# Optimization experiments

Hardware: AMD Instinct MI355X
Metric: run time of the kernel (lower is better)

## Reference

```python
import jax, jax.numpy as jnp
import numpy as np

N, E, B, D, NODE_DIM, REL = 50000, 800000, 500, 64, 6, 200
IN_FEAT = 3 * D + 2 * NODE_DIM  # 204


def _xavier(k, shape):
    fan_out, fan_in = shape
    lim = float(np.sqrt(6.0 / (fan_in + fan_out)))
    return jax.random.uniform(k, shape, jnp.float32, -lim, lim)


def setup_inputs() -> dict:
    key = jax.random.key(0)
    ks = jax.random.split(key, 8)
    x = jax.random.normal(ks[0], (N, NODE_DIM), jnp.float32)
    edge_index = jax.random.randint(ks[1], (2, E), 0, N, jnp.int32)
    edge_rel = jax.random.randint(ks[2], (E,), 0, REL, jnp.int32)
    batch = jnp.repeat(jnp.arange(B, dtype=jnp.int32), N // B)  # 100 nodes/graph
    mask = jnp.ones((E,), jnp.float32)
    edge_emb = jax.random.normal(ks[3], (REL, D), jnp.float32) * 0.02
    W0 = _xavier(ks[4], (D, IN_FEAT))
    W1 = _xavier(ks[5], (D, IN_FEAT))
    W2 = _xavier(ks[6], (D, IN_FEAT))
    b0 = jnp.zeros((D,), jnp.float32)
    b1 = jnp.zeros((D,), jnp.float32)
    b2 = jnp.zeros((D,), jnp.float32)
    return {"x": x, "edge_index": edge_index, "edge_rel": edge_rel, "batch": batch,
            "mask": mask, "edge_emb": edge_emb, "W0": W0, "b0": b0, "W1": W1,
            "b1": b1, "W2": W2, "b2": b2, "num_graphs": B}


def reference(x, edge_index, edge_rel, batch, mask, edge_emb, W0, b0, W1, b1, W2, b2, num_graphs):
    n_nodes = x.shape[0]
    row, col = edge_index[0], edge_index[1]
    # head/tail idxs: cumulative offsets of per-graph node counts
    num_per = jax.ops.segment_sum(jnp.ones_like(batch, jnp.float32), batch, num_segments=num_graphs)
    head_idxs = jnp.cumsum(jnp.concatenate([jnp.zeros(1, jnp.float32), num_per[:-1]])).astype(jnp.int32)
    tail_idxs = head_idxs + 1
    # zero x except head/tail rows
    x0 = jnp.zeros_like(x).at[head_idxs].set(x[head_idxs]).at[tail_idxs].set(x[tail_idxs])
    ea = edge_emb[edge_rel]  # [E, D]
    m = mask[:, None]
    for W, b in ((W0, b0), (W1, b1), (W2, b2)):
        agg = jax.ops.segment_sum(ea * m, col, num_segments=n_nodes)  # [N, D]
        cnt = jax.ops.segment_sum(m, col, num_segments=n_nodes)      # [N, 1]
        node_rep = jnp.concatenate([agg / (cnt + 1.0), x0], axis=1)  # [N, D+6]
        edge_rep = jnp.concatenate([node_rep[row], node_rep[col], ea], axis=-1)  # [E, 204]
        ea = jax.nn.relu(edge_rep @ W.T + b)  # PathCon edge_mlp + gnn_non_linear
    agg = jax.ops.segment_sum(ea * m, col, num_segments=n_nodes)
    cnt = jax.ops.segment_sum(m, col, num_segments=n_nodes)
    node_rep = agg / (cnt + 1.0)  # [N, D]
    pooled = jax.ops.segment_max(node_rep, batch, num_segments=num_graphs)  # 'max' readout
    graph_emb = jnp.concatenate([pooled, node_rep[head_idxs], node_rep[tail_idxs]], axis=1)
    return graph_emb, node_rep, ea
```

## Files before the change

kernel.cpp:

```cpp
#include <hip/hip_runtime.h>
#include <stdint.h>

typedef __attribute__((ext_vector_type(8))) short short8;
typedef __attribute__((ext_vector_type(4))) float f32x4;
typedef __attribute__((ext_vector_type(2))) unsigned int u32x2;

#define D_ 64
#define NODE_DIM_ 6
#define INF_ 204
#define EB 64
#define WEA_PER_LAYER 4096
#define WN_PER_LAYER 12288

__device__ __forceinline__ unsigned int f2bf(float f){
  uint32_t u = __float_as_uint(f);
  u += 0x7fffu + ((u >> 16) & 1u);
  return u >> 16;
}

__global__ void k_counts(const int* __restrict__ batch, const int* __restrict__ col,
                         int* __restrict__ counts, int* __restrict__ cnt, int N, int E){
  int i = blockIdx.x*256 + threadIdx.x;
  if (i < E) atomicAdd(&cnt[col[i]], 1);
  if (i < N) atomicAdd(&counts[batch[i]], 1);
}

__global__ void k_scans(const int* __restrict__ cnt, int* __restrict__ off, int Nn,
                        const int* __restrict__ counts, int* __restrict__ head, int B){
  __shared__ int s[1024];
  int t = threadIdx.x;
  const int CH = (Nn + 1024) / 1024;
  int base = t*CH;
  int sum = 0;
  for (int i = 0; i < CH; ++i){ int idx = base+i; if (idx < Nn) sum += cnt[idx]; }
  s[t] = sum;
  __syncthreads();
  for (int o = 1; o < 1024; o <<= 1){
    int u = (t >= o) ? s[t-o] : 0;
    __syncthreads();
    s[t] += u;
    __syncthreads();
  }
  int run = (t == 0) ? 0 : s[t-1];
  for (int i = 0; i < CH; ++i){
    int idx = base+i;
    if (idx <= Nn){ off[idx] = run; if (idx < Nn) run += cnt[idx]; }
  }
  __syncthreads();
  int v = (t < B) ? counts[t] : 0;
  s[t] = v;
  __syncthreads();
  for (int o = 1; o < 1024; o <<= 1){
    int u = (t >= o) ? s[t-o] : 0;
    __syncthreads();
    s[t] += u;
    __syncthreads();
  }
  if (t < B) head[t] = s[t] - v;
}

__global__ void k_fill(const int* __restrict__ row, const int* __restrict__ col,
                       const int* __restrict__ rel, const float* __restrict__ mask,
                       const int* __restrict__ off, int* __restrict__ fpos,
                       int* __restrict__ csr, int* __restrict__ rowp, int* __restrict__ colp,
                       int* __restrict__ relp, float* __restrict__ maskp, int E){
  int e = blockIdx.x*256 + threadIdx.x;
  if (e >= E) return;
  int c = col[e];
  int p = atomicAdd(&fpos[c], 1);
  int pos = off[c] + p;
  csr[pos]  = e;
  rowp[pos] = row[e];
  colp[pos] = c;
  relp[pos] = rel[e];
  maskp[pos]= mask[e];
}

__global__ void k_x0b(const int* __restrict__ head, const float* __restrict__ x,
                      float* __restrict__ x0b, int B){
  int idx = blockIdx.x*256 + threadIdx.x;
  if (idx >= B*2*NODE_DIM_) return;
  int g = idx / (2*NODE_DIM_);
  int j = idx % (2*NODE_DIM_);
  int node = head[g] + j / NODE_DIM_;
  int c = j % NODE_DIM_;
  x0b[(size_t)node*8 + c] = x[node*NODE_DIM_ + c];
}

__global__ void k_pack_w(const float* __restrict__ W0, const float* __restrict__ W1,
                         const float* __restrict__ W2,
                         unsigned short* __restrict__ Wea, unsigned short* __restrict__ Wn){
  int idx = blockIdx.x*256 + threadIdx.x;
  if (idx < 3*WEA_PER_LAYER){
    int l = idx / WEA_PER_LAYER;
    int rem = idx % WEA_PER_LAYER;
    const float* W = (l==0) ? W0 : ((l==1) ? W1 : W2);
    int i = rem & 7, s = rem >> 3;
    int lane = s & 63, t = s >> 6;
    int kc = t & 1, nt = t >> 1;
    int n = lane & 15, kg = lane >> 4;
    int k = kc*32 + kg*8 + i;
    int c = nt*16 + n;
    Wea[idx] = (unsigned short)f2bf(W[c*INF_ + 140 + k]);
    return;
  }
  int idx2 = idx - 3*WEA_PER_LAYER;
  if (idx2 >= 3*WN_PER_LAYER) return;
  int l = idx2 / WN_PER_LAYER;
  int rem = idx2 % WN_PER_LAYER;
  const float* W = (l==0) ? W0 : ((l==1) ? W1 : W2);
  int i = rem & 7, s = rem >> 3;
  int lane = s & 63, t = s >> 6;
  int kc = t % 3, nt = t / 3;
  int n = lane & 15, kg = lane >> 4;
  int k = kc*32 + kg*8 + i;
  int c = nt*16 + n;
  float v = 0.f;
  if (k < 70) v = (nt < 4) ? W[c*INF_ + k] : W[(c-64)*INF_ + 70 + k];
  Wn[idx2] = (unsigned short)f2bf(v);
}

__global__ void k_pack_emb(const float* __restrict__ emb, unsigned short* __restrict__ emb_bf, int n){
  int i = blockIdx.x*256 + threadIdx.x;
  if (i < n) emb_bf[i] = (unsigned short)f2bf(emb[i]);
}

__global__ __launch_bounds__(256) void k_agg0_inv(
    const float* __restrict__ emb, const int* __restrict__ relp,
    const int* __restrict__ off, const float* __restrict__ maskp,
    float* __restrict__ agg, float* __restrict__ inv, int Nn)
{
  int wid = (blockIdx.x*256 + threadIdx.x) >> 6;
  if (wid >= Nn) return;
  int lane = threadIdx.x & 63;
  int sub = lane >> 4, q = lane & 15;
  int s = off[wid], t = off[wid+1];
  float a0=0.f,a1=0.f,a2=0.f,a3=0.f, cs=0.f;
  for (int i = s; i < t; i += 4){
    int ii = i + sub;
    float mv = (ii < t) ? maskp[ii] : 0.f;
    int r = (ii < t) ? relp[ii] : 0;
    f32x4 v = *reinterpret_cast<const f32x4*>(&emb[r*D_ + q*4]);
    a0 += v.x*mv; a1 += v.y*mv; a2 += v.z*mv; a3 += v.w*mv;
    cs += mv;
  }
  a0 += __shfl_xor(a0,16); a1 += __shfl_xor(a1,16); a2 += __shfl_xor(a2,16);
  a3 += __shfl_xor(a3,16); cs += __shfl_xor(cs,16);
  a0 += __shfl_xor(a0,32); a1 += __shfl_xor(a1,32); a2 += __shfl_xor(a2,32);
  a3 += __shfl_xor(a3,32); cs += __shfl_xor(cs,32);
  if (sub == 0){
    float iv = 1.f/(cs + 1.f);
    f32x4 w = {a0*iv, a1*iv, a2*iv, a3*iv};
    *reinterpret_cast<f32x4*>(&agg[(size_t)wid*D_ + q*4]) = w;
    if (q == 0) inv[wid] = iv;
  }
}

__global__ __launch_bounds__(256) void k_ynode(
    const float* __restrict__ agg, const float* __restrict__ x0b,
    const unsigned short* __restrict__ Wn,
    const float* __restrict__ bias, float* __restrict__ Ybuf, int Nn)
{
  __shared__ __align__(16) short tile[32*104];
  int tid = threadIdx.x;
  int n0 = blockIdx.x*32;
  if (tid < 128){
    int e = tid >> 2, w = tid & 3;
    *reinterpret_cast<short8*>(&tile[e*104 + 72 + w*8]) = short8{0,0,0,0,0,0,0,0};
  }
  const f32x4* agg4 = reinterpret_cast<const f32x4*>(agg);
  const f32x4* x0b4 = reinterpret_cast<const f32x4*>(x0b);
  for (int s = tid; s < 32*18; s += 256){
    int e = s/18, q = s - e*18;
    f32x4 v = {0.f,0.f,0.f,0.f};
    if (n0 + e < Nn){
      if (q < 16) v = agg4[(size_t)(n0+e)*16 + q];
      else        v = x0b4[(size_t)(n0+e)*2 + (q-16)];
    }
    u32x2 pk;
    pk.x = f2bf(v.x) | (f2bf(v.y) << 16);
    pk.y = f2bf(v.z) | (f2bf(v.w) << 16);
    *reinterpret_cast<u32x2*>(&tile[e*104 + q*4]) = pk;
  }
  __syncthreads();
  int lane = tid & 63, wv = tid >> 6;
  int r16 = lane & 15, kg = lane >> 4;
  const short8* W8 = reinterpret_cast<const short8*>(Wn);
  f32x4 acc[2][2] = {};
  #pragma unroll
  for (int kc = 0; kc < 3; ++kc){
    short8 a0 = *reinterpret_cast<const short8*>(&tile[r16*104 + kc*32 + kg*8]);
    short8 a1 = *reinterpret_cast<const short8*>(&tile[(16+r16)*104 + kc*32 + kg*8]);
    #pragma unroll
    for (int t = 0; t < 2; ++t){
      int nt = wv*2 + t;
      short8 wf = W8[(nt*3 + kc)*64 + lane];
      acc[0][t] = __builtin_amdgcn_mfma_f32_16x16x32_bf16(a0, wf, acc[0][t], 0,0,0);
      acc[1][t] = __builtin_amdgcn_mfma_f32_16x16x32_bf16(a1, wf, acc[1][t], 0,0,0);
    }
  }
  #pragma unroll
  for (int t = 0; t < 2; ++t){
    int nt = wv*2 + t;
    int c = nt*16 + r16;
    float b = (nt < 4) ? bias[c] : 0.f;
    #pragma unroll
    for (int m = 0; m < 2; ++m)
      #pragma unroll
      for (int j = 0; j < 4; ++j){
        int node = n0 + m*16 + kg*4 + j;
        if (node < Nn) Ybuf[(size_t)node*128 + c] = acc[m][t][j] + b;
      }
  }
}

template<int FIRST, int FOUT>
__global__ __launch_bounds__(256) void k_gemm(
    const unsigned short* __restrict__ ea_bf, const unsigned short* __restrict__ emb_bf,
    const float* __restrict__ Ybuf,
    unsigned short* __restrict__ ea_out_bf, float* __restrict__ ea_out_f32,
    float* __restrict__ agg,
    const int* __restrict__ rowp, const int* __restrict__ colp,
    const int* __restrict__ relp, const int* __restrict__ csr,
    const float* __restrict__ maskp, const float* __restrict__ inv,
    const unsigned short* __restrict__ Wea, int E)
{
  __shared__ __align__(16) float stile[EB*68];
  __shared__ int s_row[EB], s_col[EB], s_rel[EB], s_csr[EB];
  __shared__ float s_mask[EB], s_inv[EB];
  int tid = threadIdx.x;
  int e0 = blockIdx.x*EB;
  if (tid < EB){
    int ge = e0 + tid;
    bool ok = ge < E;
    int cc = ok ? colp[ge] : 0;
    s_col[tid] = cc;
    s_row[tid] = ok ? rowp[ge] : 0;
    s_mask[tid]= ok ? maskp[ge] : 0.f;
    s_inv[tid] = inv[cc];
    if (FIRST) s_rel[tid] = ok ? relp[ge] : 0;
    if (FOUT)  s_csr[tid] = ok ? csr[ge] : 0;
  }
  __syncthreads();
  const f32x4* Yb4 = reinterpret_cast<const f32x4*>(Ybuf);
  f32x4* st4 = reinterpret_cast<f32x4*>(stile);
  #pragma unroll
  for (int h = 0; h < 4; ++h){
    int s = tid + h*256;
    int e = s >> 4, q = s & 15;
    f32x4 a = Yb4[(size_t)s_row[e]*32 + q];
    f32x4 b = Yb4[(size_t)s_col[e]*32 + 16 + q];
    st4[e*17 + q] = a + b;
  }
  int lane = tid & 63, wv = tid >> 6;
  int r16 = lane & 15, kg = lane >> 4;
  const short8* W8 = reinterpret_cast<const short8*>(Wea);
  short8 wf[4][2];
  #pragma unroll
  for (int nt = 0; nt < 4; ++nt)
    #pragma unroll
    for (int kc = 0; kc < 2; ++kc)
      wf[nt][kc] = W8[(nt*2 + kc)*64 + lane];
  f32x4 acc[4] = {};
  #pragma unroll
  for (int kc = 0; kc < 2; ++kc){
    short8 a;
    if (FIRST){
      a = *reinterpret_cast<const short8*>(&emb_bf[(size_t)s_rel[wv*16 + r16]*D_ + kc*32 + kg*8]);
    } else {
      int eA = e0 + wv*16 + r16; if (eA >= E) eA = E-1;
      a = *reinterpret_cast<const short8*>(&ea_bf[(size_t)eA*D_ + kc*32 + kg*8]);
    }
    #pragma unroll
    for (int nt = 0; nt < 4; ++nt)
      acc[nt] = __builtin_amdgcn_mfma_f32_16x16x32_bf16(a, wf[nt][kc], acc[nt], 0,0,0);
  }
  __syncthreads();
  float v[4][4];
  #pragma unroll
  for (int nt = 0; nt < 4; ++nt)
    #pragma unroll
    for (int j = 0; j < 4; ++j){
      int et = wv*16 + kg*4 + j;
      float x = acc[nt][j] + stile[et*68 + nt*16 + r16];
      v[nt][j] = x > 0.f ? x : 0.f;
    }
  __syncthreads();
  if (FOUT == 0){
    unsigned short* ob = reinterpret_cast<unsigned short*>(stile);
    #pragma unroll
    for (int nt = 0; nt < 4; ++nt)
      #pragma unroll
      for (int j = 0; j < 4; ++j)
        ob[(wv*16 + kg*4 + j)*72 + nt*16 + r16] = (unsigned short)f2bf(v[nt][j]);
    __syncthreads();
    #pragma unroll
    for (int h = 0; h < 2; ++h){
      int s = tid + h*256;
      int e = s >> 3, w = s & 7;
      int ge = e0 + e;
      if (ge < E)
        *reinterpret_cast<short8*>(&ea_out_bf[(size_t)ge*D_ + w*8]) =
          *reinterpret_cast<const short8*>(&ob[e*72 + w*8]);
    }
    {
      int c = tid & 63, g = tid >> 6;
      int base = g*16;
      int cur = s_col[base]; float civ = s_inv[base]; float run = 0.f;
      #pragma unroll
      for (int e = base; e < base+16; ++e){
        int col = s_col[e];
        if (col != cur){
          atomicAdd(&agg[(size_t)cur*D_ + c], run*civ);
          run = 0.f; cur = col; civ = s_inv[e];
        }
        float val = __uint_as_float((uint32_t)ob[e*72 + c] << 16);
        run += val * s_mask[e];
      }
      atomicAdd(&agg[(size_t)cur*D_ + c], run*civ);
    }
  } else {
    #pragma unroll
    for (int nt = 0; nt < 4; ++nt)
      #pragma unroll
      for (int j = 0; j < 4; ++j)
        stile[(wv*16 + kg*4 + j)*68 + nt*16 + r16] = v[nt][j];
    __syncthreads();
    f32x4* out4 = reinterpret_cast<f32x4*>(ea_out_f32);
    #pragma unroll
    for (int h = 0; h < 4; ++h){
      int s = tid + h*256;
      int e = s >> 4, q = s & 15;
      int ge = e0 + e;
      if (ge < E) out4[(size_t)s_csr[e]*16 + q] = st4[e*17 + q];
    }
    {
      int c = tid & 63, g = tid >> 6;
      int base = g*16;
      int cur = s_col[base]; float civ = s_inv[base]; float run = 0.f;
      #pragma unroll
      for (int e = base; e < base+16; ++e){
        int col = s_col[e];
        if (col != cur){
          atomicAdd(&agg[(size_t)cur*D_ + c], run*civ);
          run = 0.f; cur = col; civ = s_inv[e];
        }
        run += stile[e*68 + c] * s_mask[e];
      }
      atomicAdd(&agg[(size_t)cur*D_ + c], run*civ);
    }
  }
}

__global__ void k_pool(const float* __restrict__ nrep_out, const int* __restrict__ head,
                       const int* __restrict__ counts, float* __restrict__ gout, int B){
  __shared__ float s[4][64];
  int g = blockIdx.x;
  int lane = threadIdx.x & 63, sub = threadIdx.x >> 6;
  int h = head[g]; int n = counts[g];
  float m = -3.402823466e38f;
  for (int i = sub; i < n; i += 4)
    m = fmaxf(m, nrep_out[(size_t)(h+i)*D_ + lane]);
  s[sub][lane] = m;
  __syncthreads();
  if (sub == 0){
    m = fmaxf(fmaxf(s[0][lane], s[1][lane]), fmaxf(s[2][lane], s[3][lane]));
    gout[(size_t)g*192 + lane]       = m;
    gout[(size_t)g*192 + 64  + lane] = nrep_out[(size_t)h*D_ + lane];
    gout[(size_t)g*192 + 128 + lane] = nrep_out[(size_t)(h+1)*D_ + lane];
  }
}

extern "C" void kernel_launch(void* const* d_in, const int* in_sizes, int n_in,
                              void* d_out, int out_size, void* d_ws, size_t ws_size,
                              hipStream_t stream)
{
  const float* x    = (const float*)d_in[0];
  const int*   eidx = (const int*)d_in[1];
  const int*   erel = (const int*)d_in[2];
  const int*   batch= (const int*)d_in[3];
  const float* mask = (const float*)d_in[4];
  const float* emb  = (const float*)d_in[5];
  const float* W0   = (const float*)d_in[6];
  const float* b0   = (const float*)d_in[7];
  const float* W1   = (const float*)d_in[8];
  const float* b1   = (const float*)d_in[9];
  const float* W2   = (const float*)d_in[10];
  const float* b2   = (const float*)d_in[11];

  int N = in_sizes[0] / NODE_DIM_;
  int E = in_sizes[2];
  int B = (int)(((long long)out_size - (long long)N*D_ - (long long)E*D_) / 192);

  float* out_ge   = (float*)d_out;
  float* out_nrep = out_ge + (size_t)B*192;
  float* out_ea   = out_nrep + (size_t)N*D_;

  char* w = (char*)d_ws;
  auto alloc = [&](size_t bytes)->char*{ char* p = w; w += (bytes + 255) & ~(size_t)255; return p; };
  unsigned short* ea_p = (unsigned short*)alloc((size_t)E*D_*2);
  float* Ybuf   = (float*)alloc((size_t)N*128*4);
  float* aggP   = (float*)alloc((size_t)N*D_*4);
  float* aggQ   = (float*)alloc((size_t)N*D_*4);
  float* x0b    = (float*)alloc((size_t)N*8*4);
  float* invb   = (float*)alloc((size_t)N*4);
  int*   cnt_i  = (int*)  alloc((size_t)N*4);
  int*   off    = (int*)  alloc((size_t)(N+1)*4);
  int*   fpos   = (int*)  alloc((size_t)N*4);
  int*   csr    = (int*)  alloc((size_t)E*4);
  int*   rowp   = (int*)  alloc((size_t)E*4);
  int*   colp   = (int*)  alloc((size_t)E*4);
  int*   relp   = (int*)  alloc((size_t)E*4);
  float* maskp  = (float*)alloc((size_t)E*4);
  int*   counts = (int*)  alloc((size_t)B*4);
  int*   head   = (int*)  alloc((size_t)B*4);
  unsigned short* Wea = (unsigned short*)alloc((size_t)3*WEA_PER_LAYER*2);
  unsigned short* Wn  = (unsigned short*)alloc((size_t)3*WN_PER_LAYER*2);
  unsigned short* emb_bf = (unsigned short*)alloc((size_t)200*D_*2 + 256);

  hipMemsetAsync(cnt_i,  0, (size_t)N*4, stream);
  hipMemsetAsync(fpos,   0, (size_t)N*4, stream);
  hipMemsetAsync(counts, 0, (size_t)B*4, stream);
  hipMemsetAsync(x0b,    0, (size_t)N*8*4, stream);
  hipMemsetAsync(aggQ,   0, (size_t)N*D_*4, stream);

  const int* erow = eidx;
  const int* ecol = eidx + E;

  k_counts   <<<(E+255)/256, 256, 0, stream>>>(batch, ecol, counts, cnt_i, N, E);
  k_scans    <<<1, 1024, 0, stream>>>(cnt_i, off, N, counts, head, B);
  k_x0b      <<<(B*2*NODE_DIM_+255)/256, 256, 0, stream>>>(head, x, x0b, B);
  k_fill     <<<(E+255)/256, 256, 0, stream>>>(erow, ecol, erel, mask, off, fpos,
                                               csr, rowp, colp, relp, maskp, E);
  k_pack_w   <<<(3*(WEA_PER_LAYER+WN_PER_LAYER)+255)/256, 256, 0, stream>>>(W0, W1, W2, Wea, Wn);
  k_pack_emb <<<(200*D_+255)/256, 256, 0, stream>>>(emb, emb_bf, 200*D_);

  int nblk_g = (E + EB - 1) / EB;
  int nblk_a = (N + 3) / 4;
  int nblk_y = (N + 31) / 32;

  k_agg0_inv<<<nblk_a, 256, 0, stream>>>(emb, relp, off, maskp, aggP, invb, N);
  k_ynode<<<nblk_y, 256, 0, stream>>>(aggP, x0b, Wn, b0, Ybuf, N);
  k_gemm<1,0><<<nblk_g, 256, 0, stream>>>(ea_p, emb_bf, Ybuf, ea_p, out_ea, aggQ,
                                          rowp, colp, relp, csr, maskp, invb, Wea, E);
  hipMemsetAsync(aggP, 0, (size_t)N*D_*4, stream);
  k_ynode<<<nblk_y, 256, 0, stream>>>(aggQ, x0b, Wn + WN_PER_LAYER, b1, Ybuf, N);
  k_gemm<0,0><<<nblk_g, 256, 0, stream>>>(ea_p, emb_bf, Ybuf, ea_p, out_ea, aggP,
                                          rowp, colp, relp, csr, maskp, invb,
                                          Wea + WEA_PER_LAYER, E);
  hipMemsetAsync(out_nrep, 0, (size_t)N*D_*4, stream);
  k_ynode<<<nblk_y, 256, 0, stream>>>(aggP, x0b, Wn + 2*WN_PER_LAYER, b2, Ybuf, N);
  k_gemm<0,1><<<nblk_g, 256, 0, stream>>>(ea_p, emb_bf, Ybuf, ea_p, out_ea, out_nrep,
                                          rowp, colp, relp, csr, maskp, invb,
                                          Wea + 2*WEA_PER_LAYER, E);

  k_pool<<<B, 256, 0, stream>>>(out_nrep, head, counts, out_ge, B);
}
```

Measured before the change: 785.1 us.

## Pack per-edge CSR metadata into int4 records and merge small setup kernels

```diff
diff --git a/kernel.cpp b/kernel.cpp
--- a/kernel.cpp
+++ b/kernel.cpp
@@ -26,7 +26,8 @@
 }
 
 __global__ void k_scans(const int* __restrict__ cnt, int* __restrict__ off, int Nn,
-                        const int* __restrict__ counts, int* __restrict__ head, int B){
+                        const int* __restrict__ counts, int* __restrict__ head, int B,
+                        const float* __restrict__ x, float* __restrict__ x0b){
   __shared__ int s[1024];
   int t = threadIdx.x;
   const int CH = (Nn + 1024) / 1024;
@@ -57,39 +58,30 @@
     __syncthreads();
   }
   if (t < B) head[t] = s[t] - v;
+  __syncthreads();
+  for (int idx = t; idx < B*2*NODE_DIM_; idx += 1024){
+    int g = idx / (2*NODE_DIM_);
+    int j = idx % (2*NODE_DIM_);
+    int node = (s[g] - counts[g]) + j / NODE_DIM_;
+    int c = j % NODE_DIM_;
+    x0b[(size_t)node*8 + c] = x[node*NODE_DIM_ + c];
+  }
 }
 
 __global__ void k_fill(const int* __restrict__ row, const int* __restrict__ col,
                        const int* __restrict__ rel, const float* __restrict__ mask,
-                       const int* __restrict__ off, int* __restrict__ fpos,
-                       int* __restrict__ csr, int* __restrict__ rowp, int* __restrict__ colp,
-                       int* __restrict__ relp, float* __restrict__ maskp, int E){
+                       int* __restrict__ fpos, int4* __restrict__ e4, int E){
   int e = blockIdx.x*256 + threadIdx.x;
   if (e >= E) return;
   int c = col[e];
-  int p = atomicAdd(&fpos[c], 1);
-  int pos = off[c] + p;
-  csr[pos]  = e;
-  rowp[pos] = row[e];
-  colp[pos] = c;
-  relp[pos] = rel[e];
-  maskp[pos]= mask[e];
-}
-
-__global__ void k_x0b(const int* __restrict__ head, const float* __restrict__ x,
-                      float* __restrict__ x0b, int B){
-  int idx = blockIdx.x*256 + threadIdx.x;
-  if (idx >= B*2*NODE_DIM_) return;
-  int g = idx / (2*NODE_DIM_);
-  int j = idx % (2*NODE_DIM_);
-  int node = head[g] + j / NODE_DIM_;
-  int c = j % NODE_DIM_;
-  x0b[(size_t)node*8 + c] = x[node*NODE_DIM_ + c];
-}
-
-__global__ void k_pack_w(const float* __restrict__ W0, const float* __restrict__ W1,
-                         const float* __restrict__ W2,
-                         unsigned short* __restrict__ Wea, unsigned short* __restrict__ Wn){
+  int pos = atomicAdd(&fpos[c], 1);
+  e4[pos] = make_int4(row[e], c, (e << 8) | rel[e], __float_as_int(mask[e]));
+}
+
+__global__ void k_pack(const float* __restrict__ W0, const float* __restrict__ W1,
+                       const float* __restrict__ W2, const float* __restrict__ emb,
+                       unsigned short* __restrict__ Wea, unsigned short* __restrict__ Wn,
+                       unsigned short* __restrict__ emb_bf){
   int idx = blockIdx.x*256 + threadIdx.x;
   if (idx < 3*WEA_PER_LAYER){
     int l = idx / WEA_PER_LAYER;
@@ -105,42 +97,41 @@
     return;
   }
   int idx2 = idx - 3*WEA_PER_LAYER;
-  if (idx2 >= 3*WN_PER_LAYER) return;
-  int l = idx2 / WN_PER_LAYER;
-  int rem = idx2 % WN_PER_LAYER;
-  const float* W = (l==0) ? W0 : ((l==1) ? W1 : W2);
-  int i = rem & 7, s = rem >> 3;
-  int lane = s & 63, t = s >> 6;
-  int kc = t % 3, nt = t / 3;
-  int n = lane & 15, kg = lane >> 4;
-  int k = kc*32 + kg*8 + i;
-  int c = nt*16 + n;
-  float v = 0.f;
-  if (k < 70) v = (nt < 4) ? W[c*INF_ + k] : W[(c-64)*INF_ + 70 + k];
-  Wn[idx2] = (unsigned short)f2bf(v);
-}
-
-__global__ void k_pack_emb(const float* __restrict__ emb, unsigned short* __restrict__ emb_bf, int n){
-  int i = blockIdx.x*256 + threadIdx.x;
-  if (i < n) emb_bf[i] = (unsigned short)f2bf(emb[i]);
+  if (idx2 < 3*WN_PER_LAYER){
+    int l = idx2 / WN_PER_LAYER;
+    int rem = idx2 % WN_PER_LAYER;
+    const float* W = (l==0) ? W0 : ((l==1) ? W1 : W2);
+    int i = rem & 7, s = rem >> 3;
+    int lane = s & 63, t = s >> 6;
+    int kc = t % 3, nt = t / 3;
+    int n = lane & 15, kg = lane >> 4;
+    int k = kc*32 + kg*8 + i;
+    int c = nt*16 + n;
+    float v = 0.f;
+    if (k < 70) v = (nt < 4) ? W[c*INF_ + k] : W[(c-64)*INF_ + 70 + k];
+    Wn[idx2] = (unsigned short)f2bf(v);
+    return;
+  }
+  int idx3 = idx2 - 3*WN_PER_LAYER;
+  if (idx3 < 200*D_) emb_bf[idx3] = (unsigned short)f2bf(emb[idx3]);
 }
 
 __global__ __launch_bounds__(256) void k_agg0_inv(
-    const float* __restrict__ emb, const int* __restrict__ relp,
-    const int* __restrict__ off, const float* __restrict__ maskp,
-    float* __restrict__ agg, float* __restrict__ inv, int Nn)
+    const float* __restrict__ emb, const int4* __restrict__ e4,
+    const int* __restrict__ off, float* __restrict__ agg,
+    float* __restrict__ inv, int Nn)
 {
   int wid = (blockIdx.x*256 + threadIdx.x) >> 6;
   if (wid >= Nn) return;
   int lane = threadIdx.x & 63;
-  int sub = lane >> 4, q = lane & 15;
+  int sub = lane >> 4, ch = lane & 15;
   int s = off[wid], t = off[wid+1];
   float a0=0.f,a1=0.f,a2=0.f,a3=0.f, cs=0.f;
   for (int i = s; i < t; i += 4){
     int ii = i + sub;
-    float mv = (ii < t) ? maskp[ii] : 0.f;
-    int r = (ii < t) ? relp[ii] : 0;
-    f32x4 v = *reinterpret_cast<const f32x4*>(&emb[r*D_ + q*4]);
+    float mv = 0.f; int r = 0;
+    if (ii < t){ int4 q = e4[ii]; r = q.z & 0xff; mv = __int_as_float(q.w); }
+    f32x4 v = *reinterpret_cast<const f32x4*>(&emb[r*D_ + ch*4]);
     a0 += v.x*mv; a1 += v.y*mv; a2 += v.z*mv; a3 += v.w*mv;
     cs += mv;
   }
@@ -150,9 +141,9 @@
   a3 += __shfl_xor(a3,32); cs += __shfl_xor(cs,32);
   if (sub == 0){
     float iv = 1.f/(cs + 1.f);
-    f32x4 w = {a0*iv, a1*iv, a2*iv, a3*iv};
-    *reinterpret_cast<f32x4*>(&agg[(size_t)wid*D_ + q*4]) = w;
-    if (q == 0) inv[wid] = iv;
+    f32x4 wv = {a0*iv, a1*iv, a2*iv, a3*iv};
+    *reinterpret_cast<f32x4*>(&agg[(size_t)wid*D_ + ch*4]) = wv;
+    if (ch == 0) inv[wid] = iv;
   }
 }
 
@@ -220,9 +211,7 @@
     const float* __restrict__ Ybuf,
     unsigned short* __restrict__ ea_out_bf, float* __restrict__ ea_out_f32,
     float* __restrict__ agg,
-    const int* __restrict__ rowp, const int* __restrict__ colp,
-    const int* __restrict__ relp, const int* __restrict__ csr,
-    const float* __restrict__ maskp, const float* __restrict__ inv,
+    const int4* __restrict__ e4, const float* __restrict__ inv,
     const unsigned short* __restrict__ Wea, int E)
 {
   __shared__ __align__(16) float stile[EB*68];
@@ -232,14 +221,14 @@
   int e0 = blockIdx.x*EB;
   if (tid < EB){
     int ge = e0 + tid;
-    bool ok = ge < E;
-    int cc = ok ? colp[ge] : 0;
-    s_col[tid] = cc;
-    s_row[tid] = ok ? rowp[ge] : 0;
-    s_mask[tid]= ok ? maskp[ge] : 0.f;
-    s_inv[tid] = inv[cc];
-    if (FIRST) s_rel[tid] = ok ? relp[ge] : 0;
-    if (FOUT)  s_csr[tid] = ok ? csr[ge] : 0;
+    int4 q = {0,0,0,0};
+    if (ge < E) q = e4[ge];
+    s_row[tid] = q.x;
+    s_col[tid] = q.y;
+    s_mask[tid]= (ge < E) ? __int_as_float(q.w) : 0.f;
+    s_inv[tid] = inv[q.y];
+    if (FIRST) s_rel[tid] = q.z & 0xff;
+    if (FOUT)  s_csr[tid] = q.z >> 8;
   }
   __syncthreads();
   const f32x4* Yb4 = reinterpret_cast<const f32x4*>(Ybuf);
@@ -400,59 +389,49 @@
   auto alloc = [&](size_t bytes)->char*{ char* p = w; w += (bytes + 255) & ~(size_t)255; return p; };
   unsigned short* ea_p = (unsigned short*)alloc((size_t)E*D_*2);
   float* Ybuf   = (float*)alloc((size_t)N*128*4);
-  float* aggP   = (float*)alloc((size_t)N*D_*4);
-  float* aggQ   = (float*)alloc((size_t)N*D_*4);
+  float* aggA   = (float*)alloc((size_t)N*D_*4);
+  float* invb   = (float*)alloc((size_t)N*4);
+  float* aggB   = (float*)alloc((size_t)N*D_*4);
+  float* aggC   = (float*)alloc((size_t)N*D_*4);
+  int*   cnt_i  = (int*)  alloc((size_t)N*4);
+  int*   counts = (int*)  alloc((size_t)B*4);
   float* x0b    = (float*)alloc((size_t)N*8*4);
-  float* invb   = (float*)alloc((size_t)N*4);
-  int*   cnt_i  = (int*)  alloc((size_t)N*4);
+  size_t zspan  = (size_t)((char*)x0b + (size_t)N*8*4 - (char*)aggB);
   int*   off    = (int*)  alloc((size_t)(N+1)*4);
   int*   fpos   = (int*)  alloc((size_t)N*4);
-  int*   csr    = (int*)  alloc((size_t)E*4);
-  int*   rowp   = (int*)  alloc((size_t)E*4);
-  int*   colp   = (int*)  alloc((size_t)E*4);
-  int*   relp   = (int*)  alloc((size_t)E*4);
-  float* maskp  = (float*)alloc((size_t)E*4);
-  int*   counts = (int*)  alloc((size_t)B*4);
+  int4*  e4     = (int4*) alloc((size_t)E*16);
   int*   head   = (int*)  alloc((size_t)B*4);
   unsigned short* Wea = (unsigned short*)alloc((size_t)3*WEA_PER_LAYER*2);
   unsigned short* Wn  = (unsigned short*)alloc((size_t)3*WN_PER_LAYER*2);
   unsigned short* emb_bf = (unsigned short*)alloc((size_t)200*D_*2 + 256);
 
-  hipMemsetAsync(cnt_i,  0, (size_t)N*4, stream);
-  hipMemsetAsync(fpos,   0, (size_t)N*4, stream);
-  hipMemsetAsync(counts, 0, (size_t)B*4, stream);
-  hipMemsetAsync(x0b,    0, (size_t)N*8*4, stream);
-  hipMemsetAsync(aggQ,   0, (size_t)N*D_*4, stream);
+  hipMemsetAsync(aggB, 0, zspan, stream);
+  hipMemsetAsync(out_nrep, 0, (size_t)N*D_*4, stream);
 
   const int* erow = eidx;
   const int* ecol = eidx + E;
 
-  k_counts   <<<(E+255)/256, 256, 0, stream>>>(batch, ecol, counts, cnt_i, N, E);
-  k_scans    <<<1, 1024, 0, stream>>>(cnt_i, off, N, counts, head, B);
-  k_x0b      <<<(B*2*NODE_DIM_+255)/256, 256, 0, stream>>>(head, x, x0b, B);
-  k_fill     <<<(E+255)/256, 256, 0, stream>>>(erow, ecol, erel, mask, off, fpos,
-                                               csr, rowp, colp, relp, maskp, E);
-  k_pack_w   <<<(3*(WEA_PER_LAYER+WN_PER_LAYER)+255)/256, 256, 0, stream>>>(W0, W1, W2, Wea, Wn);
-  k_pack_emb <<<(200*D_+255)/256, 256, 0, stream>>>(emb, emb_bf, 200*D_);
+  k_counts <<<(E+255)/256, 256, 0, stream>>>(batch, ecol, counts, cnt_i, N, E);
+  k_scans  <<<1, 1024, 0, stream>>>(cnt_i, off, N, counts, head, B, x, x0b);
+  hipMemcpyAsync(fpos, off, (size_t)N*4, hipMemcpyDeviceToDevice, stream);
+  k_fill   <<<(E+255)/256, 256, 0, stream>>>(erow, ecol, erel, mask, fpos, e4, E);
+  k_pack   <<<(3*(WEA_PER_LAYER+WN_PER_LAYER)+200*D_+255)/256, 256, 0, stream>>>(
+             W0, W1, W2, emb, Wea, Wn, emb_bf);
 
   int nblk_g = (E + EB - 1) / EB;
   int nblk_a = (N + 3) / 4;
   int nblk_y = (N + 31) / 32;
 
-  k_agg0_inv<<<nblk_a, 256, 0, stream>>>(emb, relp, off, maskp, aggP, invb, N);
-  k_ynode<<<nblk_y, 256, 0, stream>>>(aggP, x0b, Wn, b0, Ybuf, N);
-  k_gemm<1,0><<<nblk_g, 256, 0, stream>>>(ea_p, emb_bf, Ybuf, ea_p, out_ea, aggQ,
-                                          rowp, colp, relp, csr, maskp, invb, Wea, E);
-  hipMemsetAsync(aggP, 0, (size_t)N*D_*4, stream);
-  k_ynode<<<nblk_y, 256, 0, stream>>>(aggQ, x0b, Wn + WN_PER_LAYER, b1, Ybuf, N);
-  k_gemm<0,0><<<nblk_g, 256, 0, stream>>>(ea_p, emb_bf, Ybuf, ea_p, out_ea, aggP,
-                                          rowp, colp, relp, csr, maskp, invb,
-                                          Wea + WEA_PER_LAYER, E);
-  hipMemsetAsync(out_nrep, 0, (size_t)N*D_*4, stream);
-  k_ynode<<<nblk_y, 256, 0, stream>>>(aggP, x0b, Wn + 2*WN_PER_LAYER, b2, Ybuf, N);
+  k_agg0_inv<<<nblk_a, 256, 0, stream>>>(emb, e4, off, aggA, invb, N);
+  k_ynode<<<nblk_y, 256, 0, stream>>>(aggA, x0b, Wn, b0, Ybuf, N);
+  k_gemm<1,0><<<nblk_g, 256, 0, stream>>>(ea_p, emb_bf, Ybuf, ea_p, out_ea, aggB,
+                                          e4, invb, Wea, E);
+  k_ynode<<<nblk_y, 256, 0, stream>>>(aggB, x0b, Wn + WN_PER_LAYER, b1, Ybuf, N);
+  k_gemm<0,0><<<nblk_g, 256, 0, stream>>>(ea_p, emb_bf, Ybuf, ea_p, out_ea, aggC,
+                                          e4, invb, Wea + WEA_PER_LAYER, E);
+  k_ynode<<<nblk_y, 256, 0, stream>>>(aggC, x0b, Wn + 2*WN_PER_LAYER, b2, Ybuf, N);
   k_gemm<0,1><<<nblk_g, 256, 0, stream>>>(ea_p, emb_bf, Ybuf, ea_p, out_ea, out_nrep,
-                                          rowp, colp, relp, csr, maskp, invb,
-                                          Wea + 2*WEA_PER_LAYER, E);
+                                          e4, invb, Wea + 2*WEA_PER_LAYER, E);
 
   k_pool<<<B, 256, 0, stream>>>(out_nrep, head, counts, out_ge, B);
 }
```

Result: faster. 733.6 us (-6.6%).
